# Kernel optimization log

Hardware: AMD Instinct MI355X
Metric: run time of the kernel (lower is better)

Reference implementation:

```python
import jax, jax.numpy as jnp
import numpy as np

E, H, I, T = 8, 1024, 2816, 512
E4M3_MAX = 448.0  # torch.finfo(float8_e4m3fn).max


def _quantize_to_fp8(w):
    # per-tensor dynamic scaling, identical to quantize_to_fp8 in the source
    amax = jnp.max(jnp.abs(w))
    scale = jnp.maximum(amax / E4M3_MAX, 1e-12)
    fp8 = (w / scale).astype(jnp.float8_e4m3fn)
    return fp8, scale.reshape(1).astype(jnp.float32)


def setup_inputs() -> dict:
    key = jax.random.key(0)
    k1, k2, k3, k4 = jax.random.split(key, 4)
    x = jax.random.normal(k1, (T, H), jnp.float32)
    expert_idx = jax.random.randint(k2, (T,), 0, E)
    # learned 3D expert params (stored compressed as fp8 + per-tensor scale)
    w_gu = jax.random.normal(k3, (E, 2 * I, H), jnp.float32) * 0.02
    w_d = jax.random.normal(k4, (E, H, I), jnp.float32) * 0.02
    w_gu_fp8, w_gu_scale = _quantize_to_fp8(w_gu)
    w_d_fp8, w_d_scale = _quantize_to_fp8(w_d)
    return {
        "x": x,
        "expert_idx": expert_idx,
        "w_gu_fp8": w_gu_fp8,
        "w_gu_scale": w_gu_scale,
        "w_d_fp8": w_d_fp8,
        "w_d_scale": w_d_scale,
    }


def reference(x, expert_idx, w_gu_fp8, w_gu_scale, w_d_fp8, w_d_scale):
    # materialize(): dequantize fp8 -> high precision (fp8.to(dtype) * scale)
    w_gu = w_gu_fp8.astype(jnp.float32) * w_gu_scale  # [E, 2I, H]
    w_d = w_d_fp8.astype(jnp.float32) * w_d_scale     # [E, H, I]
    # inner experts forward: SwiGLU MLP per expert, top-1 routed tokens
    gu = jnp.einsum('th,efh->tef', x, w_gu)            # [T, E, 2I]
    gate, up = jnp.split(gu, 2, axis=-1)               # [T, E, I] each
    h = jax.nn.silu(gate) * up                          # [T, E, I]
    y = jnp.einsum('tei,ehi->teh', h, w_d)              # [T, E, H]
    out = y[jnp.arange(x.shape[0]), expert_idx]         # [T, H] select routed expert
    return out
```

## Files before the change

kernel.cpp:

```cpp
#include <hip/hip_runtime.h>
#include <hip/hip_bf16.h>
#include <stdint.h>

#define E_ 8
#define H_ 1024
#define I_ 2816
#define T_ 512

typedef __attribute__((ext_vector_type(4))) float f32x4;
typedef __attribute__((ext_vector_type(8))) short short8;

typedef __attribute__((address_space(1))) const unsigned GAS;
typedef __attribute__((address_space(3))) unsigned LAS;

__device__ __forceinline__ void dma16(const void* g, void* l) {
    __builtin_amdgcn_global_load_lds((GAS*)g, (LAS*)l, 16, 0, 0);
}
__device__ __forceinline__ unsigned short f2bf(float f) {
    return __builtin_bit_cast(unsigned short, __float2bfloat16(f));
}
__device__ __forceinline__ uint32_t pack_rne(float lo, float hi) {
    return (uint32_t)f2bf(lo) | ((uint32_t)f2bf(hi) << 16);
}
__device__ __forceinline__ uint32_t pack_trunc(float lo, float hi) {
    return (__builtin_bit_cast(uint32_t, hi) & 0xFFFF0000u) |
           (__builtin_bit_cast(uint32_t, lo) >> 16);
}

__global__ __launch_bounds__(512) void routek(const int* __restrict__ idx,
                                              int* __restrict__ counts,
                                              int* __restrict__ bucket) {
    int tid = threadIdx.x;
    if (tid < E_) counts[tid] = 0;
    for (int i = tid; i < E_ * T_; i += 512) bucket[i] = 0;
    __syncthreads();
    int e = idx[tid];
    int pos = atomicAdd(counts + e, 1);
    bucket[e * T_ + pos] = tid;
}

__global__ __launch_bounds__(256) void gemm1(const float* __restrict__ x,
                                             const float* __restrict__ wgu,
                                             const float* __restrict__ sgu_p,
                                             const int* __restrict__ counts,
                                             const int* __restrict__ bucket,
                                             __hip_bfloat16* __restrict__ hbuf) {
    int e = blockIdx.x >> 1, mt = blockIdx.x & 1;
    int cnt = counts[e];
    if (mt * 64 >= cnt) return;
    int f0 = blockIdx.y * 32;

    __shared__ __align__(16) char smem[48 * 1024 + 256];
    int* tok = (int*)(smem + 48 * 1024);

    int tid = threadIdx.x;
    int w = tid >> 6, lane = tid & 63;
    int r16 = lane & 15, kg = lane >> 4;

    const char* wg_e = (const char*)(wgu + (size_t)e * 2 * (size_t)I_ * H_);
    const char* srcB[4];
    char* dstB[4];
#pragma unroll
    for (int i = 0; i < 4; ++i) {
        int U = (w * 4 + i) * 64 + lane;
        int row = U >> 4, slot = U & 15;
        int wr = (row < 32) ? (f0 + row) : (I_ + f0 + row - 32);
        srcB[i] = wg_e + (size_t)wr * 4096 + (size_t)((slot ^ (row & 15)) * 16);
        dstB[i] = smem + 16 * 1024 + (w * 4 + i) * 1024;
    }
#pragma unroll
    for (int i = 0; i < 4; ++i) dma16(srcB[i], dstB[i]);

    if (tid < 64) tok[tid] = bucket[e * T_ + mt * 64 + tid];
    __syncthreads();

    int arow = tid >> 2, apart = tid & 3;
    const float* srcA = x + (size_t)tok[arow] * H_ + apart * 16;
    int awoff0 = (arow * 128 + apart * 32) ^ ((arow & 7) << 4);
    int awoff1 = (arow * 128 + apart * 32 + 16) ^ ((arow & 7) << 4);
    {
        float4 a0 = *(const float4*)(srcA), a1 = *(const float4*)(srcA + 4);
        float4 a2 = *(const float4*)(srcA + 8), a3 = *(const float4*)(srcA + 12);
        uint4 o0 = make_uint4(pack_rne(a0.x, a0.y), pack_rne(a0.z, a0.w),
                              pack_rne(a1.x, a1.y), pack_rne(a1.z, a1.w));
        uint4 o1 = make_uint4(pack_rne(a2.x, a2.y), pack_rne(a2.z, a2.w),
                              pack_rne(a3.x, a3.y), pack_rne(a3.z, a3.w));
        *(uint4*)(smem + awoff0) = o0;
        *(uint4*)(smem + awoff1) = o1;
    }
    __syncthreads();

    f32x4 acc[4];
#pragma unroll
    for (int m = 0; m < 4; ++m) acc[m] = (f32x4){0, 0, 0, 0};
    const float sgu = sgu_p[0];

    for (int t = 0; t < 16; ++t) {
        int cur = t & 1;
        char* Ab = smem + cur * 8192;
        char* Bb = smem + 16384 + cur * 16384;
        float4 pa0, pa1, pa2, pa3;
        if (t < 15) {
            int ns = cur ^ 1;
#pragma unroll
            for (int i = 0; i < 4; ++i)
                dma16(srcB[i] + (size_t)(t + 1) * 256, dstB[i] + ns * 16384);
            const float* s = srcA + (size_t)(t + 1) * 64;
            pa0 = *(const float4*)(s);      pa1 = *(const float4*)(s + 4);
            pa2 = *(const float4*)(s + 8);  pa3 = *(const float4*)(s + 12);
        }
#pragma unroll
        for (int kk = 0; kk < 2; ++kk) {
            int brow = w * 16 + r16;
            int bo = brow * 256 + kk * 128 + kg * 32;
            int sw = (brow & 15) << 4;
            float4 b0 = *(float4*)(Bb + (bo ^ sw));
            float4 b1 = *(float4*)(Bb + ((bo + 16) ^ sw));
            uint4 bu = make_uint4(pack_trunc(b0.x, b0.y), pack_trunc(b0.z, b0.w),
                                  pack_trunc(b1.x, b1.y), pack_trunc(b1.z, b1.w));
            short8 B = __builtin_bit_cast(short8, bu);
#pragma unroll
            for (int m = 0; m < 4; ++m) {
                int ar = m * 16 + r16;
                short8 A = *(short8*)(Ab + ((ar * 128 + kk * 64 + kg * 16) ^ ((ar & 7) << 4)));
                acc[m] = __builtin_amdgcn_mfma_f32_16x16x32_bf16(A, B, acc[m], 0, 0, 0);
            }
        }
        if (t < 15) {
            char* An = smem + (cur ^ 1) * 8192;
            uint4 o0 = make_uint4(pack_rne(pa0.x, pa0.y), pack_rne(pa0.z, pa0.w),
                                  pack_rne(pa1.x, pa1.y), pack_rne(pa1.z, pa1.w));
            uint4 o1 = make_uint4(pack_rne(pa2.x, pa2.y), pack_rne(pa2.z, pa2.w),
                                  pack_rne(pa3.x, pa3.y), pack_rne(pa3.z, pa3.w));
            *(uint4*)(An + awoff0) = o0;
            *(uint4*)(An + awoff1) = o1;
        }
        __syncthreads();
    }

    float* ex = (float*)smem;
    if (w >= 2) {
        float* dst = ex + (w - 2) * 1024;
#pragma unroll
        for (int m = 0; m < 4; ++m)
#pragma unroll
            for (int j = 0; j < 4; ++j)
                dst[(m * 16 + kg * 4 + j) * 16 + r16] = acc[m][j] * sgu;
    }
    __syncthreads();
    if (w < 2) {
        const float* src = ex + w * 1024;
#pragma unroll
        for (int m = 0; m < 4; ++m)
#pragma unroll
            for (int j = 0; j < 4; ++j) {
                int tr = m * 16 + kg * 4 + j;
                int pos = mt * 64 + tr;
                if (pos < cnt) {
                    float g = acc[m][j] * sgu;
                    float u = src[tr * 16 + r16];
                    float hv = (g / (1.f + __expf(-g))) * u;
                    hbuf[(size_t)tok[tr] * I_ + f0 + w * 16 + r16] = __float2bfloat16(hv);
                }
            }
    }
}

__global__ __launch_bounds__(256) void gemm2(const __hip_bfloat16* __restrict__ hbuf,
                                             const float* __restrict__ wd,
                                             const float* __restrict__ sd_p,
                                             const int* __restrict__ counts,
                                             const int* __restrict__ bucket,
                                             float* __restrict__ out) {
    int e = blockIdx.x >> 1, mt = blockIdx.x & 1;
    int cnt = counts[e];
    if (mt * 64 >= cnt) return;
    int h0 = blockIdx.y * 16;

    __shared__ __align__(16) char smem[48 * 1024 + 256];
    int* tok = (int*)(smem + 48 * 1024);
    int tid = threadIdx.x;
    int w = tid >> 6, lane = tid & 63;
    int r16 = lane & 15, kg = lane >> 4;

    if (tid < 64) tok[tid] = bucket[e * T_ + mt * 64 + tid];
    __syncthreads();

    const char* hb = (const char*)hbuf;
    const char* srcA[4]; char* dstA[4];
#pragma unroll
    for (int i = 0; i < 4; ++i) {
        int U = (w * 4 + i) * 64 + lane;
        int row = U >> 4, slot = U & 15;
        srcA[i] = hb + ((size_t)tok[row] * I_) * 2 + (size_t)((slot ^ (row & 15)) * 16);
        dstA[i] = smem + (w * 4 + i) * 1024;
    }
    const char* wd_e = (const char*)(wd + (size_t)e * (size_t)H_ * I_);
    const char* srcB[2]; char* dstB[2];
#pragma unroll
    for (int i = 0; i < 2; ++i) {
        int U = (w * 2 + i) * 64 + lane;
        int row = U >> 5, slot = U & 31;
        srcB[i] = wd_e + (size_t)(h0 + row) * ((size_t)I_ * 4) + (size_t)((slot ^ (row & 15)) * 16);
        dstB[i] = smem + 32 * 1024 + (w * 2 + i) * 1024;
    }
#pragma unroll
    for (int i = 0; i < 4; ++i) dma16(srcA[i], dstA[i]);
#pragma unroll
    for (int i = 0; i < 2; ++i) dma16(srcB[i], dstB[i]);
    __syncthreads();

    f32x4 acc = (f32x4){0, 0, 0, 0};
    const float sd = sd_p[0];

    for (int t = 0; t < 22; ++t) {
        int cur = t & 1;
        char* Ab = smem + cur * 16384;
        char* Bb = smem + 32768 + cur * 8192;
        if (t < 21) {
            int ns = cur ^ 1;
#pragma unroll
            for (int i = 0; i < 4; ++i)
                dma16(srcA[i] + (size_t)(t + 1) * 256, dstA[i] + ns * 16384);
#pragma unroll
            for (int i = 0; i < 2; ++i)
                dma16(srcB[i] + (size_t)(t + 1) * 512, dstB[i] + ns * 8192);
        }
#pragma unroll
        for (int kk = 0; kk < 4; ++kk) {
            int bo = r16 * 512 + kk * 128 + kg * 32;
            int sw = (r16 & 15) << 4;
            float4 b0 = *(float4*)(Bb + (bo ^ sw));
            float4 b1 = *(float4*)(Bb + ((bo + 16) ^ sw));
            uint4 bu = make_uint4(pack_trunc(b0.x, b0.y), pack_trunc(b0.z, b0.w),
                                  pack_trunc(b1.x, b1.y), pack_trunc(b1.z, b1.w));
            short8 B = __builtin_bit_cast(short8, bu);
            int ar = w * 16 + r16;
            short8 A = *(short8*)(Ab + ((ar * 256 + kk * 64 + kg * 16) ^ ((ar & 15) << 4)));
            acc = __builtin_amdgcn_mfma_f32_16x16x32_bf16(A, B, acc, 0, 0, 0);
        }
        __syncthreads();
    }
#pragma unroll
    for (int j = 0; j < 4; ++j) {
        int tr = w * 16 + kg * 4 + j;
        int pos = mt * 64 + tr;
        if (pos < cnt)
            out[(size_t)tok[tr] * H_ + h0 + r16] = acc[j] * sd;
    }
}

extern "C" void kernel_launch(void* const* d_in, const int* in_sizes, int n_in,
                              void* d_out, int out_size, void* d_ws, size_t ws_size,
                              hipStream_t stream) {
    const float* x    = (const float*)d_in[0];
    const int*   eidx = (const int*)d_in[1];
    const float* wgu  = (const float*)d_in[2];
    const float* sgu  = (const float*)d_in[3];
    const float* wd   = (const float*)d_in[4];
    const float* sd   = (const float*)d_in[5];
    float* out = (float*)d_out;

    char* ws = (char*)d_ws;
    int* counts = (int*)ws;
    int* bucket = (int*)(ws + 1024);
    __hip_bfloat16* hbuf = (__hip_bfloat16*)(ws + 32768);

    routek<<<1, 512, 0, stream>>>(eidx, counts, bucket);
    gemm1<<<dim3(E_ * 2, I_ / 32), 256, 0, stream>>>(x, wgu, sgu, counts, bucket, hbuf);
    gemm2<<<dim3(E_ * 2, H_ / 16), 256, 0, stream>>>(hbuf, wd, sd, counts, bucket, out);
}
```

Measured before the change: 124.0 us.

## Pre-convert x to bf16 and triple-buffer async LDS loads in both GEMMs

The routing kernel now also converts x to bf16 in a workspace buffer, so gemm1 can DMA its A tile straight into LDS instead of loading fp32 through registers and packing it. Both GEMMs move from double to triple buffering with two stages in flight. They use a partial vmcnt wait plus a raw barrier instead of a full __syncthreads each iteration. This is meant to hide global-load latency and remove the per-iteration A conversion, at the cost of more LDS per block (which may lower occupancy) and an extra bf16 copy of x.

```diff
diff --git a/kernel.cpp b/kernel.cpp
--- a/kernel.cpp
+++ b/kernel.cpp
@@ -27,19 +27,36 @@
            (__builtin_bit_cast(uint32_t, lo) >> 16);
 }
 
-__global__ __launch_bounds__(512) void routek(const int* __restrict__ idx,
-                                              int* __restrict__ counts,
-                                              int* __restrict__ bucket) {
+#define VM6() asm volatile("s_waitcnt vmcnt(6)" ::: "memory")
+#define VM0() asm volatile("s_waitcnt vmcnt(0)" ::: "memory")
+
+__global__ __launch_bounds__(256) void route_cvt(const float* __restrict__ x,
+                                                 const int* __restrict__ idx,
+                                                 int* __restrict__ counts,
+                                                 int* __restrict__ bucket,
+                                                 unsigned short* __restrict__ xg) {
     int tid = threadIdx.x;
-    if (tid < E_) counts[tid] = 0;
-    for (int i = tid; i < E_ * T_; i += 512) bucket[i] = 0;
-    __syncthreads();
-    int e = idx[tid];
-    int pos = atomicAdd(counts + e, 1);
-    bucket[e * T_ + pos] = tid;
-}
-
-__global__ __launch_bounds__(256) void gemm1(const float* __restrict__ x,
+    if (blockIdx.x == 0) {
+        if (tid < E_) counts[tid] = 0;
+        for (int i = tid; i < E_ * T_; i += 256) bucket[i] = 0;
+        __syncthreads();
+#pragma unroll
+        for (int k = 0; k < 2; ++k) {
+            int t = tid + k * 256;
+            int e = idx[t];
+            int pos = atomicAdd(counts + e, 1);
+            bucket[e * T_ + pos] = t;
+        }
+    }
+    int unit = blockIdx.x * 256 + tid;
+    const float* xp = x + (size_t)unit * 8;
+    float4 a = *(const float4*)xp, b = *(const float4*)(xp + 4);
+    uint4 o = make_uint4(pack_rne(a.x, a.y), pack_rne(a.z, a.w),
+                         pack_rne(b.x, b.y), pack_rne(b.z, b.w));
+    *(uint4*)(xg + (size_t)unit * 8) = o;
+}
+
+__global__ __launch_bounds__(256) void gemm1(const unsigned short* __restrict__ xg,
                                              const float* __restrict__ wgu,
                                              const float* __restrict__ sgu_p,
                                              const int* __restrict__ counts,
@@ -50,70 +67,64 @@
     if (mt * 64 >= cnt) return;
     int f0 = blockIdx.y * 32;
 
-    __shared__ __align__(16) char smem[48 * 1024 + 256];
-    int* tok = (int*)(smem + 48 * 1024);
-
-    int tid = threadIdx.x;
-    int w = tid >> 6, lane = tid & 63;
+    __shared__ __align__(16) char smem[72 * 1024 + 256];
+    int* tok = (int*)(smem + 72 * 1024);
+    int tid = threadIdx.x, w = tid >> 6, lane = tid & 63;
     int r16 = lane & 15, kg = lane >> 4;
 
+    float sgu = sgu_p[0];
+    asm volatile("" :: "v"(sgu));
+
+    if (tid < 64) tok[tid] = bucket[e * T_ + mt * 64 + tid];
+    __syncthreads();
+
+    const char* xb = (const char*)xg;
+    const char* srcA[2]; char* dstA[2];
+#pragma unroll
+    for (int i = 0; i < 2; ++i) {
+        int U = (w * 2 + i) * 64 + lane;
+        int row = U >> 3, sl = U & 7;
+        srcA[i] = xb + (size_t)tok[row] * 2048 + (size_t)((sl ^ (row & 7)) * 16);
+        dstA[i] = smem + (w * 2 + i) * 1024;
+    }
     const char* wg_e = (const char*)(wgu + (size_t)e * 2 * (size_t)I_ * H_);
-    const char* srcB[4];
-    char* dstB[4];
+    const char* srcB[4]; char* dstB[4];
 #pragma unroll
     for (int i = 0; i < 4; ++i) {
         int U = (w * 4 + i) * 64 + lane;
-        int row = U >> 4, slot = U & 15;
+        int row = U >> 4, sl = U & 15;
         int wr = (row < 32) ? (f0 + row) : (I_ + f0 + row - 32);
-        srcB[i] = wg_e + (size_t)wr * 4096 + (size_t)((slot ^ (row & 15)) * 16);
-        dstB[i] = smem + 16 * 1024 + (w * 4 + i) * 1024;
-    }
-#pragma unroll
-    for (int i = 0; i < 4; ++i) dma16(srcB[i], dstB[i]);
-
-    if (tid < 64) tok[tid] = bucket[e * T_ + mt * 64 + tid];
-    __syncthreads();
-
-    int arow = tid >> 2, apart = tid & 3;
-    const float* srcA = x + (size_t)tok[arow] * H_ + apart * 16;
-    int awoff0 = (arow * 128 + apart * 32) ^ ((arow & 7) << 4);
-    int awoff1 = (arow * 128 + apart * 32 + 16) ^ ((arow & 7) << 4);
-    {
-        float4 a0 = *(const float4*)(srcA), a1 = *(const float4*)(srcA + 4);
-        float4 a2 = *(const float4*)(srcA + 8), a3 = *(const float4*)(srcA + 12);
-        uint4 o0 = make_uint4(pack_rne(a0.x, a0.y), pack_rne(a0.z, a0.w),
-                              pack_rne(a1.x, a1.y), pack_rne(a1.z, a1.w));
-        uint4 o1 = make_uint4(pack_rne(a2.x, a2.y), pack_rne(a2.z, a2.w),
-                              pack_rne(a3.x, a3.y), pack_rne(a3.z, a3.w));
-        *(uint4*)(smem + awoff0) = o0;
-        *(uint4*)(smem + awoff1) = o1;
-    }
-    __syncthreads();
+        srcB[i] = wg_e + (size_t)wr * 4096 + (size_t)((sl ^ (row & 15)) * 16);
+        dstB[i] = smem + 24 * 1024 + (w * 4 + i) * 1024;
+    }
+
+#define G1_ISSUE(s, buf)                                                     \
+    do {                                                                     \
+        _Pragma("unroll")                                                    \
+        for (int i = 0; i < 2; ++i) dma16(srcA[i] + (size_t)(s) * 128, dstA[i] + (buf) * 8192);  \
+        _Pragma("unroll")                                                    \
+        for (int i = 0; i < 4; ++i) dma16(srcB[i] + (size_t)(s) * 256, dstB[i] + (buf) * 16384); \
+    } while (0)
+
+    G1_ISSUE(0, 0);
+    G1_ISSUE(1, 1);
 
     f32x4 acc[4];
 #pragma unroll
     for (int m = 0; m < 4; ++m) acc[m] = (f32x4){0, 0, 0, 0};
-    const float sgu = sgu_p[0];
 
     for (int t = 0; t < 16; ++t) {
-        int cur = t & 1;
-        char* Ab = smem + cur * 8192;
-        char* Bb = smem + 16384 + cur * 16384;
-        float4 pa0, pa1, pa2, pa3;
-        if (t < 15) {
-            int ns = cur ^ 1;
-#pragma unroll
-            for (int i = 0; i < 4; ++i)
-                dma16(srcB[i] + (size_t)(t + 1) * 256, dstB[i] + ns * 16384);
-            const float* s = srcA + (size_t)(t + 1) * 64;
-            pa0 = *(const float4*)(s);      pa1 = *(const float4*)(s + 4);
-            pa2 = *(const float4*)(s + 8);  pa3 = *(const float4*)(s + 12);
-        }
+        VM6();
+        __builtin_amdgcn_s_barrier();
+        int tp = (t + 2 < 16) ? t + 2 : 15;
+        G1_ISSUE(tp, (t + 2) % 3);
+        const char* Ab = smem + (t % 3) * 8192;
+        const char* Bb = smem + 24 * 1024 + (t % 3) * 16384;
 #pragma unroll
         for (int kk = 0; kk < 2; ++kk) {
             int brow = w * 16 + r16;
             int bo = brow * 256 + kk * 128 + kg * 32;
-            int sw = (brow & 15) << 4;
+            int sw = r16 << 4;
             float4 b0 = *(float4*)(Bb + (bo ^ sw));
             float4 b1 = *(float4*)(Bb + ((bo + 16) ^ sw));
             uint4 bu = make_uint4(pack_trunc(b0.x, b0.y), pack_trunc(b0.z, b0.w),
@@ -126,17 +137,9 @@
                 acc[m] = __builtin_amdgcn_mfma_f32_16x16x32_bf16(A, B, acc[m], 0, 0, 0);
             }
         }
-        if (t < 15) {
-            char* An = smem + (cur ^ 1) * 8192;
-            uint4 o0 = make_uint4(pack_rne(pa0.x, pa0.y), pack_rne(pa0.z, pa0.w),
-                                  pack_rne(pa1.x, pa1.y), pack_rne(pa1.z, pa1.w));
-            uint4 o1 = make_uint4(pack_rne(pa2.x, pa2.y), pack_rne(pa2.z, pa2.w),
-                                  pack_rne(pa3.x, pa3.y), pack_rne(pa3.z, pa3.w));
-            *(uint4*)(An + awoff0) = o0;
-            *(uint4*)(An + awoff1) = o1;
-        }
-        __syncthreads();
-    }
+    }
+    VM0();
+    __syncthreads();
 
     float* ex = (float*)smem;
     if (w >= 2) {
@@ -177,11 +180,13 @@
     if (mt * 64 >= cnt) return;
     int h0 = blockIdx.y * 16;
 
-    __shared__ __align__(16) char smem[48 * 1024 + 256];
-    int* tok = (int*)(smem + 48 * 1024);
-    int tid = threadIdx.x;
-    int w = tid >> 6, lane = tid & 63;
+    __shared__ __align__(16) char smem[72 * 1024 + 256];
+    int* tok = (int*)(smem + 72 * 1024);
+    int tid = threadIdx.x, w = tid >> 6, lane = tid & 63;
     int r16 = lane & 15, kg = lane >> 4;
+
+    float sd = sd_p[0];
+    asm volatile("" :: "v"(sd));
 
     if (tid < 64) tok[tid] = bucket[e * T_ + mt * 64 + tid];
     __syncthreads();
@@ -191,8 +196,8 @@
 #pragma unroll
     for (int i = 0; i < 4; ++i) {
         int U = (w * 4 + i) * 64 + lane;
-        int row = U >> 4, slot = U & 15;
-        srcA[i] = hb + ((size_t)tok[row] * I_) * 2 + (size_t)((slot ^ (row & 15)) * 16);
+        int row = U >> 4, sl = U & 15;
+        srcA[i] = hb + (size_t)tok[row] * (I_ * 2) + (size_t)((sl ^ (row & 15)) * 16);
         dstA[i] = smem + (w * 4 + i) * 1024;
     }
     const char* wd_e = (const char*)(wd + (size_t)e * (size_t)H_ * I_);
@@ -200,36 +205,35 @@
 #pragma unroll
     for (int i = 0; i < 2; ++i) {
         int U = (w * 2 + i) * 64 + lane;
-        int row = U >> 5, slot = U & 31;
-        srcB[i] = wd_e + (size_t)(h0 + row) * ((size_t)I_ * 4) + (size_t)((slot ^ (row & 15)) * 16);
-        dstB[i] = smem + 32 * 1024 + (w * 2 + i) * 1024;
-    }
-#pragma unroll
-    for (int i = 0; i < 4; ++i) dma16(srcA[i], dstA[i]);
-#pragma unroll
-    for (int i = 0; i < 2; ++i) dma16(srcB[i], dstB[i]);
-    __syncthreads();
+        int row = U >> 5, sl = U & 31;
+        srcB[i] = wd_e + (size_t)(h0 + row) * ((size_t)I_ * 4) + (size_t)((sl ^ (row & 15)) * 16);
+        dstB[i] = smem + 48 * 1024 + (w * 2 + i) * 1024;
+    }
+
+#define G2_ISSUE(s, buf)                                                     \
+    do {                                                                     \
+        _Pragma("unroll")                                                    \
+        for (int i = 0; i < 4; ++i) dma16(srcA[i] + (size_t)(s) * 256, dstA[i] + (buf) * 16384); \
+        _Pragma("unroll")                                                    \
+        for (int i = 0; i < 2; ++i) dma16(srcB[i] + (size_t)(s) * 512, dstB[i] + (buf) * 8192);  \
+    } while (0)
+
+    G2_ISSUE(0, 0);
+    G2_ISSUE(1, 1);
 
     f32x4 acc = (f32x4){0, 0, 0, 0};
-    const float sd = sd_p[0];
 
     for (int t = 0; t < 22; ++t) {
-        int cur = t & 1;
-        char* Ab = smem + cur * 16384;
-        char* Bb = smem + 32768 + cur * 8192;
-        if (t < 21) {
-            int ns = cur ^ 1;
-#pragma unroll
-            for (int i = 0; i < 4; ++i)
-                dma16(srcA[i] + (size_t)(t + 1) * 256, dstA[i] + ns * 16384);
-#pragma unroll
-            for (int i = 0; i < 2; ++i)
-                dma16(srcB[i] + (size_t)(t + 1) * 512, dstB[i] + ns * 8192);
-        }
+        VM6();
+        __builtin_amdgcn_s_barrier();
+        int tp = (t + 2 < 22) ? t + 2 : 21;
+        G2_ISSUE(tp, (t + 2) % 3);
+        const char* Ab = smem + (t % 3) * 16384;
+        const char* Bb = smem + 48 * 1024 + (t % 3) * 8192;
 #pragma unroll
         for (int kk = 0; kk < 4; ++kk) {
             int bo = r16 * 512 + kk * 128 + kg * 32;
-            int sw = (r16 & 15) << 4;
+            int sw = r16 << 4;
             float4 b0 = *(float4*)(Bb + (bo ^ sw));
             float4 b1 = *(float4*)(Bb + ((bo + 16) ^ sw));
             uint4 bu = make_uint4(pack_trunc(b0.x, b0.y), pack_trunc(b0.z, b0.w),
@@ -239,8 +243,9 @@
             short8 A = *(short8*)(Ab + ((ar * 256 + kk * 64 + kg * 16) ^ ((ar & 15) << 4)));
             acc = __builtin_amdgcn_mfma_f32_16x16x32_bf16(A, B, acc, 0, 0, 0);
         }
-        __syncthreads();
-    }
+    }
+    VM0();
+
 #pragma unroll
     for (int j = 0; j < 4; ++j) {
         int tr = w * 16 + kg * 4 + j;
@@ -264,9 +269,10 @@
     char* ws = (char*)d_ws;
     int* counts = (int*)ws;
     int* bucket = (int*)(ws + 1024);
-    __hip_bfloat16* hbuf = (__hip_bfloat16*)(ws + 32768);
-
-    routek<<<1, 512, 0, stream>>>(eidx, counts, bucket);
-    gemm1<<<dim3(E_ * 2, I_ / 32), 256, 0, stream>>>(x, wgu, sgu, counts, bucket, hbuf);
+    unsigned short* xg = (unsigned short*)(ws + 32768);
+    __hip_bfloat16* hbuf = (__hip_bfloat16*)(ws + 1114112);
+
+    route_cvt<<<256, 256, 0, stream>>>(x, eidx, counts, bucket, xg);
+    gemm1<<<dim3(E_ * 2, I_ / 32), 256, 0, stream>>>(xg, wgu, sgu, counts, bucket, hbuf);
     gemm2<<<dim3(E_ * 2, H_ / 16), 256, 0, stream>>>(hbuf, wd, sd, counts, bucket, out);
 }
```

Result: no change. 121.7 us (-1.8%).
